# Optimization experiments

Measured on AMD Instinct MI355X. Metric: run time of the kernel, lower is better.

## Reference

```python
import jax, jax.numpy as jnp
import numpy as np

B, S, D = 1, 4096, 2048
H, KVH, HD = 16, 2, 128  # heads, kv heads, head_dim
GROUPS = H // KVH
ROPE_THETA = 1e6


def rotate_half(x):
    x1, x2 = x[..., : HD // 2], x[..., HD // 2:]
    return jnp.concatenate((-x2, x1), axis=-1)


def setup_inputs() -> dict:
    key = jax.random.key(0)
    ks = jax.random.split(key, 8)
    std = 0.02
    return {
        "hidden_states": jax.random.normal(ks[0], (B, S, D), jnp.float32),
        "position_ids": jnp.arange(S, dtype=jnp.int64 if jax.config.jax_enable_x64 else jnp.int32)[None, :].repeat(B, 0),
        "Wq": jax.random.normal(ks[1], (D, H * HD), jnp.float32) * std,
        "bq": jax.random.normal(ks[2], (H * HD,), jnp.float32) * std,
        "Wk": jax.random.normal(ks[3], (D, KVH * HD), jnp.float32) * std,
        "bk": jax.random.normal(ks[4], (KVH * HD,), jnp.float32) * std,
        "Wv": jax.random.normal(ks[5], (D, KVH * HD), jnp.float32) * std,
        "bv": jax.random.normal(ks[6], (KVH * HD,), jnp.float32) * std,
        "Wo": jax.random.normal(ks[7], (H * HD, D), jnp.float32) * std,
    }


def reference(hidden_states, position_ids, Wq, bq, Wk, bk, Wv, bv, Wo):
    bsz, q_len, _ = hidden_states.shape
    # projections (W stored as [in, out], equivalent to torch Linear weight.T)
    q = (hidden_states @ Wq + bq).reshape(bsz, q_len, H, HD).transpose(0, 2, 1, 3)
    k = (hidden_states @ Wk + bk).reshape(bsz, q_len, KVH, HD).transpose(0, 2, 1, 3)
    v = (hidden_states @ Wv + bv).reshape(bsz, q_len, KVH, HD).transpose(0, 2, 1, 3)

    # rotary embedding cache
    inv_freq = 1.0 / (ROPE_THETA ** (jnp.arange(0, HD, 2, dtype=jnp.float32) / HD))
    t = jnp.arange(q_len, dtype=jnp.float32)
    freqs = jnp.outer(t, inv_freq)                       # [S, HD/2]
    emb = jnp.concatenate((freqs, freqs), axis=-1)       # [S, HD]
    cos = jnp.cos(emb)[position_ids][:, None]            # [B,1,S,HD]
    sin = jnp.sin(emb)[position_ids][:, None]

    q = q * cos + rotate_half(q) * sin
    k = k * cos + rotate_half(k) * sin

    # GQA: expand kv heads (repeat_interleave along head dim)
    k = jnp.repeat(k, GROUPS, axis=1)                    # [B,H,S,HD]
    v = jnp.repeat(v, GROUPS, axis=1)

    scores = jnp.einsum("bhqd,bhkd->bhqk", q, k) / np.sqrt(HD)
    attn = jax.nn.softmax(scores.astype(jnp.float32), axis=-1).astype(q.dtype)
    out = jnp.einsum("bhqk,bhkd->bhqd", attn, v)         # [B,H,S,HD]
    out = out.transpose(0, 2, 1, 3).reshape(bsz, q_len, H * HD)
    return out @ Wo
```

## Files before the change

### kernel.cpp

```cpp
#include <hip/hip_runtime.h>

typedef unsigned short ushort_t;
typedef unsigned int u32;
typedef __attribute__((ext_vector_type(8))) short bf16x8;
typedef __attribute__((ext_vector_type(4))) float f32x4;
typedef __attribute__((ext_vector_type(16))) float f32x16;
typedef __attribute__((ext_vector_type(4))) unsigned int u32x4;

#define AS3(p) ((__attribute__((address_space(3))) unsigned int*)(p))
#define AS1(p) ((const __attribute__((address_space(1))) unsigned int*)(p))

__device__ __forceinline__ void gl_lds16(const void* g, void* l) {
  __builtin_amdgcn_global_load_lds(AS1(g), AS3(l), 16, 0, 0);
}

__device__ __forceinline__ ushort_t f2bf(float f) {
  unsigned u = __float_as_uint(f);
  u += 0x7FFFu + ((u >> 16) & 1u);
  return (ushort_t)(u >> 16);
}

__device__ __forceinline__ u32 cvtpk(float a, float b) {
  u32 r;
  asm("v_cvt_pk_bf16_f32 %0, %1, %2" : "=v"(r) : "v"(a), "v"(b));
  return r;
}


__global__ void k_rope(const int* __restrict__ pid, float2* __restrict__ tab) {
  int t = blockIdx.x * 256 + threadIdx.x;
  int s = t >> 6, j = t & 63;
  double inv = pow(1000000.0, -(double)j / 64.0);
  double a = (double)pid[s] * inv;
  tab[t] = make_float2((float)cos(a), (float)sin(a));
}

__global__ void k_cvt(const float* __restrict__ in, unsigned char* __restrict__ out) {
  int i = blockIdx.x * 256 + threadIdx.x;
  float4 v = ((const float4*)in)[i];
  ushort_t r[4] = { f2bf(v.x), f2bf(v.y), f2bf(v.z), f2bf(v.w) };
  *(ulonglong1*)(out + (size_t)i * 8) = *(ulonglong1*)r;
}

__global__ void k_transpose(const float* __restrict__ W, unsigned char* __restrict__ outT, int N) {
  __shared__ float tile[32][33];
  int n0 = blockIdx.x * 32, k0 = blockIdx.y * 32;
  int tx = threadIdx.x & 31, ty = threadIdx.x >> 5;
  #pragma unroll
  for (int i = 0; i < 4; ++i)
    tile[ty + i * 8][tx] = W[(size_t)(k0 + ty + i * 8) * N + n0 + tx];
  __syncthreads();
  #pragma unroll
  for (int i = 0; i < 4; ++i) {
    int n = ty + i * 8;
    *(ushort_t*)(outT + ((size_t)(n0 + n) * 2048 + k0 + tx) * 2) = f2bf(tile[tx][n]);
  }
}

__device__ __forceinline__ void gemm_loop(
    const unsigned char* __restrict__ aSrc0,
    const unsigned char* __restrict__ bSrc0,
    unsigned char* ldsA, unsigned char* ldsB,
    f32x4 acc[2][8])
{
  const int tid = threadIdx.x;
  const int lane = tid & 63, wave = tid >> 6;
  const int c = lane & 15, g = lane >> 4;

  int rowS[4], swzS[4];
  #pragma unroll
  for (int i = 0; i < 4; ++i) {
    int o = (i * 4 + wave) * 1024 + lane * 16;
    int row = o >> 7, slot = (o >> 4) & 7;
    rowS[i] = row;
    swzS[i] = (slot ^ (row & 7)) << 4;
  }
  #pragma unroll
  for (int mi = 0; mi < 2; ++mi)
    for (int nj = 0; nj < 8; ++nj)
      for (int q = 0; q < 4; ++q) acc[mi][nj][q] = 0.0f;

  for (int kt = 0; kt < 32; ++kt) {
    __syncthreads();
    #pragma unroll
    for (int i = 0; i < 4; ++i) {
      gl_lds16(aSrc0 + (size_t)rowS[i] * 4096 + kt * 128 + swzS[i], ldsA + (i * 4 + wave) * 1024);
      gl_lds16(bSrc0 + (size_t)rowS[i] * 4096 + kt * 128 + swzS[i], ldsB + (i * 4 + wave) * 1024);
    }
    __syncthreads();
    #pragma unroll
    for (int ks = 0; ks < 2; ++ks) {
      bf16x8 a[2];
      #pragma unroll
      for (int mi = 0; mi < 2; ++mi) {
        int row = wave * 32 + mi * 16 + c;
        a[mi] = *(const bf16x8*)(ldsA + row * 128 + (((ks * 4 + g) ^ (row & 7)) << 4));
      }
      #pragma unroll
      for (int nj = 0; nj < 8; ++nj) {
        int row = nj * 16 + c;
        bf16x8 b = *(const bf16x8*)(ldsB + row * 128 + (((ks * 4 + g) ^ (row & 7)) << 4));
        acc[0][nj] = __builtin_amdgcn_mfma_f32_16x16x32_bf16(a[0], b, acc[0][nj], 0, 0, 0);
        acc[1][nj] = __builtin_amdgcn_mfma_f32_16x16x32_bf16(a[1], b, acc[1][nj], 0, 0, 0);
      }
    }
  }
}


__global__ __launch_bounds__(256, 2) void k_qkv_gemm(
    const unsigned char* __restrict__ hidB, const unsigned char* __restrict__ wT,
    const float* __restrict__ bq, const float* __restrict__ bk, const float* __restrict__ bv,
    const float2* __restrict__ rope,
    unsigned char* __restrict__ Qs, unsigned char* __restrict__ Ks, unsigned char* __restrict__ VTs)
{
  __shared__ alignas(16) unsigned char lds[32768];
  const int bx = blockIdx.x;
  const int swz = (bx & 7) * 80 + (bx >> 3);
  const int bm = swz / 20, bn = swz % 20;
  f32x4 acc[2][8];
  gemm_loop(hidB + (size_t)bm * 128 * 4096, wT + (size_t)bn * 128 * 4096, lds, lds + 16384, acc);

  const int lane = threadIdx.x & 63, wave = threadIdx.x >> 6;
  const int c = lane & 15, g = lane >> 4;
  const int n0 = bn * 128;
  float bias[8];
  #pragma unroll
  for (int nj = 0; nj < 8; ++nj) {
    int n = n0 + nj * 16 + c;
    bias[nj] = (n < 2048) ? bq[n] : (n < 2304 ? bk[n - 2048] : bv[n - 2304]);
  }
  const int m0 = bm * 128 + wave * 32;
  if (n0 < 2304) {
    constexpr float SCALE_Q = 0.08838834764831845f * 1.4426950408889634f;
    const bool isQ = (n0 < 2048);
    unsigned char* out = isQ ? (Qs + (size_t)(n0 >> 7) * 4096 * 256)
                             : (Ks + (size_t)((n0 - 2048) >> 7) * 4096 * 256);
    const float scl = isQ ? SCALE_Q : 1.0f;
    #pragma unroll
    for (int mi = 0; mi < 2; ++mi)
      #pragma unroll
      for (int r = 0; r < 4; ++r) {
        int srow = m0 + mi * 16 + g * 4 + r;
        #pragma unroll
        for (int nj = 0; nj < 4; ++nj) {
          int d = nj * 16 + c;
          float2 cs = rope[srow * 64 + d];
          float x1 = acc[mi][nj][r] + bias[nj];
          float x2 = acc[mi][nj + 4][r] + bias[nj + 4];
          float o1 = (x1 * cs.x - x2 * cs.y) * scl;
          float o2 = (x2 * cs.x + x1 * cs.y) * scl;
          *(ushort_t*)(out + (size_t)srow * 256 + d * 2) = f2bf(o1);
          *(ushort_t*)(out + (size_t)srow * 256 + (d + 64) * 2) = f2bf(o2);
        }
      }
  } else {
    unsigned char* out = VTs + (size_t)((n0 - 2304) >> 7) * 128 * 8192;
    #pragma unroll
    for (int mi = 0; mi < 2; ++mi)
      #pragma unroll
      for (int r = 0; r < 4; ++r) {
        int srow = m0 + mi * 16 + g * 4 + r;
        #pragma unroll
        for (int nj = 0; nj < 8; ++nj) {
          int d = nj * 16 + c;
          *(ushort_t*)(out + (size_t)d * 8192 + srow * 2) = f2bf(acc[mi][nj][r] + bias[nj]);
        }
      }
  }
}


__global__ __launch_bounds__(256, 2) void k_attn(
    const unsigned char* __restrict__ Qs, const unsigned char* __restrict__ Ks,
    const unsigned char* __restrict__ VTs, unsigned char* __restrict__ AO)
{
  __shared__ alignas(16) unsigned char lds[65536];
  const int tid = threadIdx.x, lane = tid & 63, wave = tid >> 6;
  const int l31 = lane & 31, hi = lane >> 5;
  const int qt = blockIdx.x, h = blockIdx.y, kvh = h >> 3;

  bf16x8 qv[8];
  const unsigned char* qbase = Qs + ((size_t)h * 4096 + qt * 128 + wave * 32 + l31) * 256;
  #pragma unroll
  for (int dks = 0; dks < 8; ++dks)
    qv[dks] = *(const bf16x8*)(qbase + dks * 32 + hi * 16);

  f32x16 o[4];
  #pragma unroll
  for (int dn = 0; dn < 4; ++dn)
    #pragma unroll
    for (int r = 0; r < 16; ++r) o[dn][r] = 0.0f;
  float lsum = 0.0f;

  const unsigned char* kbase = Ks + (size_t)kvh * 4096 * 256;
  const unsigned char* vbase = VTs + (size_t)kvh * 128 * 8192;

  int kRow[4], kSwz[4];
  size_t vOff[4];
  #pragma unroll
  for (int i = 0; i < 4; ++i) {
    int o_ = (i * 4 + wave) * 1024 + lane * 16;
    int row = o_ >> 8, slot = (o_ >> 4) & 15;
    int sw = slot ^ (row & 15);
    kRow[i] = row; kSwz[i] = sw << 4;
    int d = row + ((sw >> 3) << 6);
    vOff[i] = (size_t)d * 8192 + (sw & 7) * 16;
  }

  auto STAGE = [&](int t, int b) {
    const unsigned char* kst = kbase + (size_t)t * 16384;
    const unsigned char* vst = vbase + (size_t)t * 128;
    unsigned char* dK = lds + b * 16384;
    unsigned char* dV = lds + 32768 + b * 16384;
    #pragma unroll
    for (int i = 0; i < 4; ++i) {
      gl_lds16(kst + kRow[i] * 256 + kSwz[i], dK + (i * 4 + wave) * 1024);
      gl_lds16(vst + vOff[i], dV + (i * 4 + wave) * 1024);
    }
  };

  STAGE(0, 0);
  __syncthreads();

  for (int t = 0; t < 64; ++t) {
    const int cur = t & 1;
    if (t < 63) STAGE(t + 1, cur ^ 1);

    const unsigned char* Kb = lds + cur * 16384;
    const unsigned char* Vb = lds + 32768 + cur * 16384;

    f32x16 sA, sB;
    #pragma unroll
    for (int r = 0; r < 16; ++r) { sA[r] = 0.0f; sB[r] = 0.0f; }
    __builtin_amdgcn_s_setprio(1);
    #pragma unroll
    for (int dks = 0; dks < 8; ++dks) {
      int sl = (((dks << 1) | hi) ^ (l31 & 15)) << 4;
      bf16x8 k0 = *(const bf16x8*)(Kb + l31 * 256 + sl);
      bf16x8 k1 = *(const bf16x8*)(Kb + (32 + l31) * 256 + sl);
      sA = __builtin_amdgcn_mfma_f32_32x32x16_bf16(k0, qv[dks], sA, 0, 0, 0);
      sB = __builtin_amdgcn_mfma_f32_32x32x16_bf16(k1, qv[dks], sB, 0, 0, 0);
    }
    __builtin_amdgcn_s_setprio(0);

    #pragma unroll
    for (int r = 0; r < 16; ++r) { sA[r] = exp2f(sA[r]); sB[r] = exp2f(sB[r]); }
    float t0 = (sA[0] + sA[1]) + (sA[2] + sA[3]);
    float t1 = (sA[4] + sA[5]) + (sA[6] + sA[7]);
    float t2 = (sA[8] + sA[9]) + (sA[10] + sA[11]);
    float t3 = (sA[12] + sA[13]) + (sA[14] + sA[15]);
    float t4 = (sB[0] + sB[1]) + (sB[2] + sB[3]);
    float t5 = (sB[4] + sB[5]) + (sB[6] + sB[7]);
    float t6 = (sB[8] + sB[9]) + (sB[10] + sB[11]);
    float t7 = (sB[12] + sB[13]) + (sB[14] + sB[15]);
    lsum += ((t0 + t1) + (t2 + t3)) + ((t4 + t5) + (t6 + t7));

    bf16x8 pa[4];
    #pragma unroll
    for (int half = 0; half < 2; ++half) {
      const f32x16& S = half ? sB : sA;
      #pragma unroll
      for (int part = 0; part < 2; ++part) {
        int base = part * 8;
        u32 A0 = cvtpk(S[base + 0], S[base + 1]);
        u32 A1 = cvtpk(S[base + 2], S[base + 3]);
        u32 B0 = cvtpk(S[base + 4], S[base + 5]);
        u32 B1 = cvtpk(S[base + 6], S[base + 7]);
        asm volatile("v_permlane32_swap_b32 %0, %1" : "+v"(A0), "+v"(B0));
        asm volatile("v_permlane32_swap_b32 %0, %1" : "+v"(A1), "+v"(B1));
        union { u32x4 u; bf16x8 b; } cv;
        cv.u = (u32x4){A0, A1, B0, B1};
        pa[half * 2 + part] = cv.b;
      }
    }

    __builtin_amdgcn_s_setprio(1);
    #pragma unroll
    for (int ks4 = 0; ks4 < 4; ++ks4) {
      #pragma unroll
      for (int dn = 0; dn < 4; ++dn) {
        int row = ((dn & 1) << 5) + l31;
        int slotIdx = ((dn >> 1) << 3) | (ks4 << 1) | hi;
        bf16x8 vf = *(const bf16x8*)(Vb + row * 256 + ((slotIdx ^ (row & 15)) << 4));
        o[dn] = __builtin_amdgcn_mfma_f32_32x32x16_bf16(pa[ks4], vf, o[dn], 0, 0, 0);
      }
    }
    __builtin_amdgcn_s_setprio(0);

    __syncthreads();
  }

  lsum += __shfl_xor(lsum, 32);
  float inv = 1.0f / lsum;
  #pragma unroll
  for (int r = 0; r < 16; ++r) {
    int crow = (r & 3) + 8 * (r >> 2) + 4 * hi;
    float invq = __shfl(inv, (lane & 32) | crow);
    int srow = qt * 128 + wave * 32 + crow;
    #pragma unroll
    for (int dn = 0; dn < 4; ++dn)
      *(ushort_t*)(AO + ((size_t)srow * 2048 + h * 128 + dn * 32 + l31) * 2) =
          f2bf(o[dn][r] * invq);
  }
}


__global__ __launch_bounds__(256, 2) void k_out_gemm(
    const unsigned char* __restrict__ AO, const unsigned char* __restrict__ woT,
    float* __restrict__ out)
{
  __shared__ alignas(16) unsigned char lds[32768];
  const int bx = blockIdx.x;
  const int swz = (bx & 7) * 64 + (bx >> 3);
  const int bm = swz >> 4, bn = swz & 15;
  f32x4 acc[2][8];
  gemm_loop(AO + (size_t)bm * 128 * 4096, woT + (size_t)bn * 128 * 4096, lds, lds + 16384, acc);
  const int lane = threadIdx.x & 63, wave = threadIdx.x >> 6;
  const int c = lane & 15, g = lane >> 4;
  const int m0 = bm * 128 + wave * 32;
  #pragma unroll
  for (int mi = 0; mi < 2; ++mi)
    #pragma unroll
    for (int r = 0; r < 4; ++r) {
      int row = m0 + mi * 16 + g * 4 + r;
      #pragma unroll
      for (int nj = 0; nj < 8; ++nj)
        out[(size_t)row * 2048 + bn * 128 + nj * 16 + c] = acc[mi][nj][r];
    }
}


extern "C" void kernel_launch(void* const* d_in, const int* in_sizes, int n_in,
                              void* d_out, int out_size, void* d_ws, size_t ws_size,
                              hipStream_t stream) {
  const float* hidden = (const float*)d_in[0];
  const int*   pos    = (const int*)d_in[1];
  const float* Wq = (const float*)d_in[2];
  const float* bq = (const float*)d_in[3];
  const float* Wk = (const float*)d_in[4];
  const float* bk = (const float*)d_in[5];
  const float* Wv = (const float*)d_in[6];
  const float* bv = (const float*)d_in[7];
  const float* Wo = (const float*)d_in[8];
  float* out = (float*)d_out;
  unsigned char* ws = (unsigned char*)d_ws;

  float2*        rope  = (float2*)(ws + 0);
  unsigned char* hidB  = ws + 2097152;
  unsigned char* wqkvT = ws + 18874368;
  unsigned char* woT   = ws + 29360128;
  unsigned char* Qs    = ws + 37748736;
  unsigned char* Ks    = ws + 54525952;
  unsigned char* VTs   = ws + 56623104;
  unsigned char* AO    = hidB;

  k_rope<<<1024, 256, 0, stream>>>(pos, rope);
  k_cvt<<<8192, 256, 0, stream>>>(hidden, hidB);
  k_transpose<<<dim3(64, 64), 256, 0, stream>>>(Wq, wqkvT, 2048);
  k_transpose<<<dim3(8, 64), 256, 0, stream>>>(Wk, wqkvT + (size_t)2048 * 2048 * 2, 256);
  k_transpose<<<dim3(8, 64), 256, 0, stream>>>(Wv, wqkvT + (size_t)2304 * 2048 * 2, 256);
  k_transpose<<<dim3(64, 64), 256, 0, stream>>>(Wo, woT, 2048);
  k_qkv_gemm<<<640, 256, 0, stream>>>(hidB, wqkvT, bq, bk, bv, rope, Qs, Ks, VTs);
  k_attn<<<dim3(32, 16), 256, 0, stream>>>(Qs, Ks, VTs, AO);
  k_out_gemm<<<512, 256, 0, stream>>>(AO, woT, out);
}
```

Before: 274.3 us.

## Split attention KV range across two blocks and combine partials

The attention kernel now splits the 4096-key range into two halves over a third grid dimension. Each block handles half the keys with 32-key tiles and a smaller LDS footprint, and launch bounds rise to three blocks per CU. Each half writes a normalized bf16 partial output plus its row sum, and a new combine kernel mixes the two halves weighted by their sums. This raises block count and occupancy for the 512-block attention grid, at the cost of an extra pass over the attention output and a second bf16 rounding. It depends on softmax having no max subtraction, since the partials are combined with plain sums.

```diff
diff --git a/kernel.cpp b/kernel.cpp
--- a/kernel.cpp
+++ b/kernel.cpp
@@ -19,6 +19,8 @@
   u += 0x7FFFu + ((u >> 16) & 1u);
   return (ushort_t)(u >> 16);
 }
+
+__device__ __forceinline__ float bf2f(u32 hi16) { return __uint_as_float(hi16 << 16); }
 
 __device__ __forceinline__ u32 cvtpk(float a, float b) {
   u32 r;
@@ -171,14 +173,16 @@
 }
 
 
-__global__ __launch_bounds__(256, 2) void k_attn(
+__global__ __launch_bounds__(256, 3) void k_attn(
     const unsigned char* __restrict__ Qs, const unsigned char* __restrict__ Ks,
-    const unsigned char* __restrict__ VTs, unsigned char* __restrict__ AO)
-{
-  __shared__ alignas(16) unsigned char lds[65536];
+    const unsigned char* __restrict__ VTs,
+    unsigned char* __restrict__ P0, unsigned char* __restrict__ P1,
+    float* __restrict__ L0, float* __restrict__ L1)
+{
+  __shared__ alignas(16) unsigned char lds[32768];
   const int tid = threadIdx.x, lane = tid & 63, wave = tid >> 6;
   const int l31 = lane & 31, hi = lane >> 5;
-  const int qt = blockIdx.x, h = blockIdx.y, kvh = h >> 3;
+  const int qt = blockIdx.x, h = blockIdx.y, sp = blockIdx.z, kvh = h >> 3;
 
   bf16x8 qv[8];
   const unsigned char* qbase = Qs + ((size_t)h * 4096 + qt * 128 + wave * 32 + l31) * 256;
@@ -193,29 +197,28 @@
     for (int r = 0; r < 16; ++r) o[dn][r] = 0.0f;
   float lsum = 0.0f;
 
-  const unsigned char* kbase = Ks + (size_t)kvh * 4096 * 256;
-  const unsigned char* vbase = VTs + (size_t)kvh * 128 * 8192;
-
-  int kRow[4], kSwz[4];
-  size_t vOff[4];
-  #pragma unroll
-  for (int i = 0; i < 4; ++i) {
+  const unsigned char* kbase = Ks + (size_t)kvh * 4096 * 256 + (size_t)sp * 2048 * 256;
+  const unsigned char* vbase = VTs + (size_t)kvh * 128 * 8192 + (size_t)sp * 2048 * 2;
+
+  int kOff[2]; size_t vOff[2];
+  #pragma unroll
+  for (int i = 0; i < 2; ++i) {
     int o_ = (i * 4 + wave) * 1024 + lane * 16;
     int row = o_ >> 8, slot = (o_ >> 4) & 15;
     int sw = slot ^ (row & 15);
-    kRow[i] = row; kSwz[i] = sw << 4;
-    int d = row + ((sw >> 3) << 6);
-    vOff[i] = (size_t)d * 8192 + (sw & 7) * 16;
+    kOff[i] = row * 256 + sw * 16;
+    int d = ((sw >> 2) << 5) + row;
+    vOff[i] = (size_t)d * 8192 + (sw & 3) * 16;
   }
 
   auto STAGE = [&](int t, int b) {
-    const unsigned char* kst = kbase + (size_t)t * 16384;
-    const unsigned char* vst = vbase + (size_t)t * 128;
-    unsigned char* dK = lds + b * 16384;
-    unsigned char* dV = lds + 32768 + b * 16384;
-    #pragma unroll
-    for (int i = 0; i < 4; ++i) {
-      gl_lds16(kst + kRow[i] * 256 + kSwz[i], dK + (i * 4 + wave) * 1024);
+    const unsigned char* kst = kbase + (size_t)t * 8192;
+    const unsigned char* vst = vbase + (size_t)t * 64;
+    unsigned char* dK = lds + b * 8192;
+    unsigned char* dV = lds + 16384 + b * 8192;
+    #pragma unroll
+    for (int i = 0; i < 2; ++i) {
+      gl_lds16(kst + kOff[i], dK + (i * 4 + wave) * 1024);
       gl_lds16(vst + vOff[i], dV + (i * 4 + wave) * 1024);
     }
   };
@@ -227,62 +230,50 @@
     const int cur = t & 1;
     if (t < 63) STAGE(t + 1, cur ^ 1);
 
-    const unsigned char* Kb = lds + cur * 16384;
-    const unsigned char* Vb = lds + 32768 + cur * 16384;
-
-    f32x16 sA, sB;
-    #pragma unroll
-    for (int r = 0; r < 16; ++r) { sA[r] = 0.0f; sB[r] = 0.0f; }
+    const unsigned char* Kb = lds + cur * 8192;
+    const unsigned char* Vb = lds + 16384 + cur * 8192;
+
+    f32x16 sA;
+    #pragma unroll
+    for (int r = 0; r < 16; ++r) sA[r] = 0.0f;
     __builtin_amdgcn_s_setprio(1);
     #pragma unroll
     for (int dks = 0; dks < 8; ++dks) {
-      int sl = (((dks << 1) | hi) ^ (l31 & 15)) << 4;
-      bf16x8 k0 = *(const bf16x8*)(Kb + l31 * 256 + sl);
-      bf16x8 k1 = *(const bf16x8*)(Kb + (32 + l31) * 256 + sl);
+      bf16x8 k0 = *(const bf16x8*)(Kb + l31 * 256 + ((((dks << 1) | hi) ^ (l31 & 15)) << 4));
       sA = __builtin_amdgcn_mfma_f32_32x32x16_bf16(k0, qv[dks], sA, 0, 0, 0);
-      sB = __builtin_amdgcn_mfma_f32_32x32x16_bf16(k1, qv[dks], sB, 0, 0, 0);
     }
     __builtin_amdgcn_s_setprio(0);
 
     #pragma unroll
-    for (int r = 0; r < 16; ++r) { sA[r] = exp2f(sA[r]); sB[r] = exp2f(sB[r]); }
+    for (int r = 0; r < 16; ++r) sA[r] = exp2f(sA[r]);
     float t0 = (sA[0] + sA[1]) + (sA[2] + sA[3]);
     float t1 = (sA[4] + sA[5]) + (sA[6] + sA[7]);
     float t2 = (sA[8] + sA[9]) + (sA[10] + sA[11]);
     float t3 = (sA[12] + sA[13]) + (sA[14] + sA[15]);
-    float t4 = (sB[0] + sB[1]) + (sB[2] + sB[3]);
-    float t5 = (sB[4] + sB[5]) + (sB[6] + sB[7]);
-    float t6 = (sB[8] + sB[9]) + (sB[10] + sB[11]);
-    float t7 = (sB[12] + sB[13]) + (sB[14] + sB[15]);
-    lsum += ((t0 + t1) + (t2 + t3)) + ((t4 + t5) + (t6 + t7));
-
-    bf16x8 pa[4];
-    #pragma unroll
-    for (int half = 0; half < 2; ++half) {
-      const f32x16& S = half ? sB : sA;
-      #pragma unroll
-      for (int part = 0; part < 2; ++part) {
-        int base = part * 8;
-        u32 A0 = cvtpk(S[base + 0], S[base + 1]);
-        u32 A1 = cvtpk(S[base + 2], S[base + 3]);
-        u32 B0 = cvtpk(S[base + 4], S[base + 5]);
-        u32 B1 = cvtpk(S[base + 6], S[base + 7]);
-        asm volatile("v_permlane32_swap_b32 %0, %1" : "+v"(A0), "+v"(B0));
-        asm volatile("v_permlane32_swap_b32 %0, %1" : "+v"(A1), "+v"(B1));
-        union { u32x4 u; bf16x8 b; } cv;
-        cv.u = (u32x4){A0, A1, B0, B1};
-        pa[half * 2 + part] = cv.b;
-      }
+    lsum += (t0 + t1) + (t2 + t3);
+
+    bf16x8 pa[2];
+    #pragma unroll
+    for (int part = 0; part < 2; ++part) {
+      int base = part * 8;
+      u32 A0 = cvtpk(sA[base + 0], sA[base + 1]);
+      u32 A1 = cvtpk(sA[base + 2], sA[base + 3]);
+      u32 B0 = cvtpk(sA[base + 4], sA[base + 5]);
+      u32 B1 = cvtpk(sA[base + 6], sA[base + 7]);
+      asm volatile("v_permlane32_swap_b32 %0, %1" : "+v"(A0), "+v"(B0));
+      asm volatile("v_permlane32_swap_b32 %0, %1" : "+v"(A1), "+v"(B1));
+      union { u32x4 u; bf16x8 b; } cv;
+      cv.u = (u32x4){A0, A1, B0, B1};
+      pa[part] = cv.b;
     }
 
     __builtin_amdgcn_s_setprio(1);
     #pragma unroll
-    for (int ks4 = 0; ks4 < 4; ++ks4) {
+    for (int ks4 = 0; ks4 < 2; ++ks4) {
       #pragma unroll
       for (int dn = 0; dn < 4; ++dn) {
-        int row = ((dn & 1) << 5) + l31;
-        int slotIdx = ((dn >> 1) << 3) | (ks4 << 1) | hi;
-        bf16x8 vf = *(const bf16x8*)(Vb + row * 256 + ((slotIdx ^ (row & 15)) << 4));
+        int slotIdx = (dn << 2) | (ks4 << 1) | hi;
+        bf16x8 vf = *(const bf16x8*)(Vb + l31 * 256 + ((slotIdx ^ (l31 & 15)) << 4));
         o[dn] = __builtin_amdgcn_mfma_f32_32x32x16_bf16(pa[ks4], vf, o[dn], 0, 0, 0);
       }
     }
@@ -293,6 +284,7 @@
 
   lsum += __shfl_xor(lsum, 32);
   float inv = 1.0f / lsum;
+  unsigned char* P = sp ? P1 : P0;
   #pragma unroll
   for (int r = 0; r < 16; ++r) {
     int crow = (r & 3) + 8 * (r >> 2) + 4 * hi;
@@ -300,9 +292,36 @@
     int srow = qt * 128 + wave * 32 + crow;
     #pragma unroll
     for (int dn = 0; dn < 4; ++dn)
-      *(ushort_t*)(AO + ((size_t)srow * 2048 + h * 128 + dn * 32 + l31) * 2) =
+      *(ushort_t*)(P + ((size_t)srow * 2048 + h * 128 + dn * 32 + l31) * 2) =
           f2bf(o[dn][r] * invq);
   }
+  if (hi == 0) {
+    float* L = sp ? L1 : L0;
+    L[h * 4096 + qt * 128 + wave * 32 + l31] = lsum;
+  }
+}
+
+
+__global__ void k_comb(unsigned char* __restrict__ P0, const unsigned char* __restrict__ P1,
+                       const float* __restrict__ L0, const float* __restrict__ L1)
+{
+  int g = blockIdx.x * 256 + threadIdx.x;
+  u32x4 a = *(const u32x4*)(P0 + (size_t)g * 16);
+  u32x4 b = *(const u32x4*)(P1 + (size_t)g * 16);
+  int e0 = g * 8;
+  int srow = e0 >> 11, hh = (e0 >> 7) & 15;
+  float l0 = L0[hh * 4096 + srow], l1 = L1[hh * 4096 + srow];
+  float inv = 1.0f / (l0 + l1);
+  float w0 = l0 * inv, w1 = l1 * inv;
+  ushort_t r[8];
+  #pragma unroll
+  for (int j = 0; j < 4; ++j) {
+    float lo = bf2f(a[j] & 0xFFFFu) * w0 + bf2f(b[j] & 0xFFFFu) * w1;
+    float hi2 = bf2f(a[j] >> 16) * w0 + bf2f(b[j] >> 16) * w1;
+    r[2 * j] = f2bf(lo);
+    r[2 * j + 1] = f2bf(hi2);
+  }
+  *(u32x4*)(P0 + (size_t)g * 16) = *(u32x4*)r;
 }
 
 
@@ -348,12 +367,15 @@
 
   float2*        rope  = (float2*)(ws + 0);
   unsigned char* hidB  = ws + 2097152;
-  unsigned char* wqkvT = ws + 18874368;
-  unsigned char* woT   = ws + 29360128;
-  unsigned char* Qs    = ws + 37748736;
-  unsigned char* Ks    = ws + 54525952;
-  unsigned char* VTs   = ws + 56623104;
-  unsigned char* AO    = hidB;
+  unsigned char* woT   = ws + 18874368;
+  unsigned char* Qs    = ws + 27262976;
+  unsigned char* Ks    = ws + 44040192;
+  unsigned char* VTs   = ws + 46137344;
+  float*         L0    = (float*)(ws + 48234496);
+  float*         L1    = (float*)(ws + 48496640);
+  unsigned char* wqkvT = ws + 48758784;
+  unsigned char* P1    = ws + 48758784;
+  unsigned char* P0    = hidB;
 
   k_rope<<<1024, 256, 0, stream>>>(pos, rope);
   k_cvt<<<8192, 256, 0, stream>>>(hidden, hidB);
@@ -362,6 +384,7 @@
   k_transpose<<<dim3(8, 64), 256, 0, stream>>>(Wv, wqkvT + (size_t)2304 * 2048 * 2, 256);
   k_transpose<<<dim3(64, 64), 256, 0, stream>>>(Wo, woT, 2048);
   k_qkv_gemm<<<640, 256, 0, stream>>>(hidB, wqkvT, bq, bk, bv, rope, Qs, Ks, VTs);
-  k_attn<<<dim3(32, 16), 256, 0, stream>>>(Qs, Ks, VTs, AO);
-  k_out_gemm<<<512, 256, 0, stream>>>(AO, woT, out);
-}
+  k_attn<<<dim3(32, 16, 2), 256, 0, stream>>>(Qs, Ks, VTs, P0, P1, L0, L1);
+  k_comb<<<4096, 256, 0, stream>>>(P0, P1, L0, L1);
+  k_out_gemm<<<512, 256, 0, stream>>>(P0, woT, out);
+}
```

Measured after the change: 285.9 us. 4.2% more time.
